# Kernel optimization log

Hardware: AMD Instinct MI355X
Metric: run time of the kernel (lower is better)

## Reference

```python
import jax, jax.numpy as jnp
import numpy as np

EPS = 1e-06
FP8_MAX = 448.0  # float8_e4m3fn max
T, H = 8192, 4096


def setup_inputs() -> dict:
    key = jax.random.key(0)
    ks = jax.random.split(key, 5)
    return {
        "hidden_states": jax.random.normal(ks[0], (T, H), dtype=jnp.float32),
        "norm_w": jax.random.uniform(ks[1], (4, H), dtype=jnp.float32),
        "w": jax.random.uniform(ks[2], (3, H, H), dtype=jnp.float32),
        "wscale": jax.random.uniform(ks[3], (3,), dtype=jnp.float32),
        "scale": jax.random.uniform(ks[4], (3,), dtype=jnp.float32),
    }


def _rmsnorm(x, g):
    var = jnp.mean(x * x, axis=-1, keepdims=True)
    return x * jax.lax.rsqrt(var + EPS) * g


def _fp8_quant(x, s):
    # static per-tensor quant: scale, clamp to fp8 range, cast to e4m3 and back
    q = jnp.clip(x / s, -FP8_MAX, FP8_MAX)
    return q.astype(jnp.float8_e4m3fn).astype(jnp.float32)


def _fp8_linear(x, wq, s_in, s_w):
    qx = _fp8_quant(x, s_in)
    return (qx @ wq) * (s_in * s_w)


def reference(hidden_states, norm_w, w, wscale, scale):
    # weight fp8 quantization (module stores weights already in fp8)
    wq = w.astype(jnp.float8_e4m3fn).astype(jnp.float32)  # [3,H,H]

    z = jax.nn.relu(hidden_states)
    x = resid = z  # all_reduce == identity on one device
    y = _rmsnorm(x, norm_w[0])

    z2 = _fp8_linear(y, wq[0], scale[0], wscale[0])
    x2 = z2 + resid
    resid = x2
    y2 = _rmsnorm(x2, norm_w[1])

    z3 = _fp8_linear(y2, wq[1], scale[1], wscale[1])
    x3 = z3 + resid
    resid = x3
    y3 = _rmsnorm(x3, norm_w[2])

    z4 = _fp8_linear(y3, wq[2], scale[2], wscale[2])
    x4 = z4 + resid
    y4 = _rmsnorm(x4, norm_w[3])
    return y4
```

## Files before the change

### kernel.cpp

```cpp
#include <hip/hip_runtime.h>

typedef float f32x4  __attribute__((ext_vector_type(4)));
typedef float f32x16 __attribute__((ext_vector_type(16)));
typedef int   i32x4  __attribute__((ext_vector_type(4)));
typedef int   i32x8  __attribute__((ext_vector_type(8)));

#define T_DIM 8192
#define H_DIM 4096
#define SC1 0x7f7f7f7f

__device__ __forceinline__ unsigned int pack_fp8x4(float a, float b, float c, float d) {
    int v = __builtin_amdgcn_cvt_pk_fp8_f32(a, b, 0, false);
    v = __builtin_amdgcn_cvt_pk_fp8_f32(c, d, v, true);
    return (unsigned int)v;
}


__global__ __launch_bounds__(256) void wquant_kernel(
    const float* __restrict__ w, unsigned char* __restrict__ wqT)
{
    const int l  = blockIdx.z;
    const int n0 = blockIdx.x * 64;
    const int k0 = blockIdx.y * 64;
    const int tid = threadIdx.x;
    __shared__ unsigned char tile[64][68];
    const float* wl = w + (size_t)l * H_DIM * H_DIM;
#pragma unroll
    for (int p = 0; p < 4; ++p) {
        int r = p * 16 + (tid >> 4);
        int c = (tid & 15) * 4;
        f32x4 v = *(const f32x4*)(wl + (size_t)(k0 + r) * H_DIM + n0 + c);
        *(unsigned int*)&tile[r][c] = pack_fp8x4(v[0], v[1], v[2], v[3]);
    }
    __syncthreads();
    const int nl = tid >> 2;
    const int g  = tid & 3;
    unsigned int words[4];
#pragma unroll
    for (int wi = 0; wi < 4; ++wi) {
        unsigned int a = 0;
#pragma unroll
        for (int b = 0; b < 4; ++b)
            a |= (unsigned int)tile[g * 16 + wi * 4 + b][nl] << (8 * b);
        words[wi] = a;
    }
    const int bn = n0 >> 8, wc = (n0 >> 6) & 3, kt = k0 >> 6;
    const int n2 = nl >> 5;
    const int lane = (g >> 1) * 32 + (nl & 31);
    const int byte0 = (g & 1) * 16;
    const size_t off = ((((size_t)l * 16 + bn) * 64 + kt) * 4 + wc) * 2 + n2;
    unsigned char* op = wqT + off * 2048 + lane * 32 + byte0;
    uint4 ov; ov.x = words[0]; ov.y = words[1]; ov.z = words[2]; ov.w = words[3];
    *(uint4*)op = ov;
}

template <int MODE>
__global__ __launch_bounds__(256) void row_kernel(
    const float* __restrict__ in,
    float* __restrict__ resid_out,
    void* __restrict__ out,
    const float* __restrict__ g,
    const float* __restrict__ scale_p)
{
    const int row = blockIdx.x;
    const int tid = threadIdx.x;
    const float* rin = in + (size_t)row * H_DIM;
    float x[16];
    float ss = 0.0f;
#pragma unroll
    for (int j = 0; j < 4; ++j) {
        const int base = (j * 256 + tid) * 4;
        f32x4 v = *(const f32x4*)(rin + base);
        f32x4 rv;
#pragma unroll
        for (int i = 0; i < 4; ++i) {
            float t = v[i];
            if (MODE == 0) t = fmaxf(t, 0.0f);
            x[j * 4 + i] = t;
            rv[i] = t;
            ss += t * t;
        }
        if (MODE == 0)
            *(f32x4*)(resid_out + (size_t)row * H_DIM + base) = rv;
    }
#pragma unroll
    for (int off = 32; off > 0; off >>= 1)
        ss += __shfl_down(ss, off, 64);
    __shared__ float red[4];
    if ((tid & 63) == 0) red[tid >> 6] = ss;
    __syncthreads();
    const float var  = (red[0] + red[1] + red[2] + red[3]) * (1.0f / (float)H_DIM);
    const float rinv = 1.0f / sqrtf(var + 1e-6f);

    if (MODE == 2) {
        float* ro = (float*)out + (size_t)row * H_DIM;
#pragma unroll
        for (int j = 0; j < 4; ++j) {
            const int base = (j * 256 + tid) * 4;
            f32x4 gv = *(const f32x4*)(g + base);
            f32x4 ov;
#pragma unroll
            for (int i = 0; i < 4; ++i) ov[i] = (x[j * 4 + i] * rinv) * gv[i];
            *(f32x4*)(ro + base) = ov;
        }
    } else {
        const float s = scale_p[0];
        unsigned int* qo = (unsigned int*)out + (size_t)row * (H_DIM / 4);
#pragma unroll
        for (int j = 0; j < 4; ++j) {
            const int base = (j * 256 + tid) * 4;
            f32x4 gv = *(const f32x4*)(g + base);
            float q[4];
#pragma unroll
            for (int i = 0; i < 4; ++i) {
                float y = (x[j * 4 + i] * rinv) * gv[i];
                y = y / s;
                q[i] = fminf(fmaxf(y, -448.0f), 448.0f);
            }
            qo[j * 256 + tid] = pack_fp8x4(q[0], q[1], q[2], q[3]);
        }
    }
}

#define LGKM0B do { asm volatile("s_waitcnt lgkmcnt(0)" ::: "memory"); \
                    __builtin_amdgcn_s_barrier(); } while (0)

#define MM2(m, P) do {                                                          \
    acc[m][0] = __builtin_amdgcn_mfma_scale_f32_32x32x64_f8f6f4(                \
        fa[m], b##P##0, acc[m][0], 0, 0, 0, SC1, 0, SC1);                       \
    acc[m][1] = __builtin_amdgcn_mfma_scale_f32_32x32x64_f8f6f4(                \
        fa[m], b##P##1, acc[m][1], 0, 0, 0, SC1, 0, SC1);                       \
} while (0)

#define RDA(ORQ, m) do {                                                        \
    *(i32x4*)&fa[m]         = *(const i32x4*)(lds + (ORQ) + wrA + (m) * 2048 + fo0); \
    *(((i32x4*)&fa[m]) + 1) = *(const i32x4*)(lds + (ORQ) + wrA + (m) * 2048 + fo1); \
} while (0)

#define AITER(WRa, WRb, LDa, LDb, FC, FN, BUF) do {                             \
    LDa = *(const i32x4*)(gAlo + kt2);                                          \
    LDb = *(const i32x4*)(gAhi + kt2);                                          \
    kt2 += 64;                                                                  \
    b##FN##0 = *(const i32x8*)(gB0 + ktb);                                      \
    b##FN##1 = *(const i32x8*)(gB0 + ktb + 2048);                               \
    ktb += 16384;                                                               \
    *(i32x4*)(lds + (BUF) + tid16)        = WRa;                                \
    *(i32x4*)(lds + (BUF) + 8192 + tid16) = WRb;                                \
    LGKM0B;                                                                     \
    __builtin_amdgcn_s_setprio(1); MM2(0, FC); MM2(1, FC);                      \
    __builtin_amdgcn_s_setprio(0);                                              \
    RDA(BUF, 0); RDA(BUF, 1);                                                   \
    __builtin_amdgcn_s_setprio(1); MM2(2, FC); MM2(3, FC);                      \
    __builtin_amdgcn_s_setprio(0);                                              \
    RDA(BUF, 2); RDA(BUF, 3);                                                   \
} while (0)

__global__ __launch_bounds__(512, 2) void gemm_fp8_kernel(
    const unsigned char* __restrict__ A,
    const unsigned char* __restrict__ B,
    float* __restrict__ C,
    const float* __restrict__ s_in,
    const float* __restrict__ s_w)
{
    __shared__ unsigned char lds[32768];

    const float alpha = s_in[0] * s_w[0];

    const int b = blockIdx.x;
    const int local = b >> 3, chunk = b & 7;
    const int bm = (chunk & 3) * 8 + (local & 7);
    const int bn = (chunk >> 2) * 8 + (local >> 3);

    const int tid  = threadIdx.x;
    const int wave = tid >> 6;
    const int lane = tid & 63;
    const int wr   = wave >> 2;
    const int wc   = wave & 3;

    const int sw  = (lane >> 1) & 3;
    const int fo0 = (lane & 31) * 64 + ((((lane >> 5) * 2) + 0 ^ sw)) * 16;
    const int fo1 = (lane & 31) * 64 + ((((lane >> 5) * 2) + 1 ^ sw)) * 16;
    const int wrA = wr * 8192;

    const int voff = (tid >> 2) * H_DIM + ((tid & 3) ^ ((tid >> 3) & 3)) * 16;
    const unsigned char* gAlo = A + (size_t)bm * 256 * H_DIM + voff;
    const unsigned char* gAhi = gAlo + (size_t)128 * H_DIM;
    const int tid16 = tid * 16;

    const unsigned char* gB0 =
        B + ((((size_t)bn * 64) * 4 + wc) * 2) * 2048 + lane * 32;

    f32x16 acc[4][2];
#pragma unroll
    for (int m = 0; m < 4; ++m)
#pragma unroll
        for (int n = 0; n < 2; ++n)
#pragma unroll
            for (int e = 0; e < 16; ++e) acc[m][n][e] = 0.0f;

    i32x8 fa[4];
    i32x4 rXa, rXb, rYa, rYb;
    i32x8 bX0, bX1, bY0, bY1;
    int kt2, ktb;

    rXa = *(const i32x4*)(gAlo);
    rXb = *(const i32x4*)(gAhi);
    bX0 = *(const i32x8*)(gB0);
    bX1 = *(const i32x8*)(gB0 + 2048);
    rYa = *(const i32x4*)(gAlo + 64);
    rYb = *(const i32x4*)(gAhi + 64);
    *(i32x4*)(lds + tid16)        = rXa;
    *(i32x4*)(lds + 8192 + tid16) = rXb;
    LGKM0B;
    RDA(0, 0); RDA(0, 1); RDA(0, 2); RDA(0, 3);
    kt2 = 128;
    ktb = 16384;

#pragma unroll 1
    for (int it = 0; it < 31; ++it) {
        AITER(rYa, rYb, rXa, rXb, X, Y, 16384);
        AITER(rXa, rXb, rYa, rYb, Y, X, 0);
    }
    bY0 = *(const i32x8*)(gB0 + ktb);
    bY1 = *(const i32x8*)(gB0 + ktb + 2048);
    *(i32x4*)(lds + 16384 + tid16)        = rYa;
    *(i32x4*)(lds + 16384 + 8192 + tid16) = rYb;
    LGKM0B;
    __builtin_amdgcn_s_setprio(1); MM2(0, X); MM2(1, X);
    __builtin_amdgcn_s_setprio(0);
    RDA(16384, 0); RDA(16384, 1);
    __builtin_amdgcn_s_setprio(1); MM2(2, X); MM2(3, X);
    __builtin_amdgcn_s_setprio(0);
    RDA(16384, 2); RDA(16384, 3);
    MM2(0, Y); MM2(1, Y); MM2(2, Y); MM2(3, Y);

    const int lrow0 = bm * 256 + wr * 128 + 4 * (lane >> 5);
    const int lcol0 = bn * 256 + wc * 64 + (lane & 31);
#pragma unroll
    for (int m = 0; m < 4; ++m) {
#pragma unroll
        for (int n = 0; n < 2; ++n) {
#pragma unroll
            for (int e = 0; e < 16; ++e) {
                const int row = lrow0 + m * 32 + (e & 3) + 8 * (e >> 2);
                float* cp = C + (size_t)row * H_DIM + lcol0 + n * 32;
                *cp = acc[m][n][e] * alpha + *cp;
            }
        }
    }
}

extern "C" void kernel_launch(void* const* d_in, const int* in_sizes, int n_in,
                              void* d_out, int out_size, void* d_ws, size_t ws_size,
                              hipStream_t stream) {
    const float* h   = (const float*)d_in[0];
    const float* nw  = (const float*)d_in[1];
    const float* w   = (const float*)d_in[2];
    const float* wsc = (const float*)d_in[3];
    const float* sc  = (const float*)d_in[4];
    float* out = (float*)d_out;

    unsigned char* wqT = (unsigned char*)d_ws;
    unsigned char* qx  = wqT + (size_t)3 * H_DIM * H_DIM;
    float* resid = (float*)(qx + (size_t)T_DIM * H_DIM);

    const size_t WSTRIDE = (size_t)H_DIM * H_DIM;

    wquant_kernel<<<dim3(64, 64, 3), 256, 0, stream>>>(w, wqT);

    row_kernel<0><<<T_DIM, 256, 0, stream>>>(h, resid, qx, nw + 0 * H_DIM, sc + 0);
    gemm_fp8_kernel<<<512, 512, 0, stream>>>(qx, wqT + 0 * WSTRIDE, resid, sc + 0, wsc + 0);

    row_kernel<1><<<T_DIM, 256, 0, stream>>>(resid, nullptr, qx, nw + 1 * H_DIM, sc + 1);
    gemm_fp8_kernel<<<512, 512, 0, stream>>>(qx, wqT + 1 * WSTRIDE, resid, sc + 1, wsc + 1);

    row_kernel<1><<<T_DIM, 256, 0, stream>>>(resid, nullptr, qx, nw + 2 * H_DIM, sc + 2);
    gemm_fp8_kernel<<<512, 512, 0, stream>>>(qx, wqT + 2 * WSTRIDE, resid, sc + 2, wsc + 2);

    row_kernel<2><<<T_DIM, 256, 0, stream>>>(resid, nullptr, out, nw + 3 * H_DIM, nullptr);
}
```

Measured before the change: 666.6 us.

## Write activations in MFMA fragment layout and load A directly to registers

The norm+quant kernel now writes fp8 activations in a tiled layout that matches the MFMA A-fragment order (32-row blocks, 64-byte K tiles split into halves). The GEMM drops the LDS staging, barriers and swizzled shared-memory reads for A and instead loads each wave's A fragments straight from global memory, the same way B is already loaded. This removes LDS traffic and block-wide synchronisation. The cost is that A tiles shared across the four column waves are now fetched redundantly from global or L2, and there is no longer a software prefetch buffer hiding load latency.

```diff
diff --git a/kernel.cpp b/kernel.cpp
--- a/kernel.cpp
+++ b/kernel.cpp
@@ -105,7 +105,8 @@
         }
     } else {
         const float s = scale_p[0];
-        unsigned int* qo = (unsigned int*)out + (size_t)row * (H_DIM / 4);
+        unsigned int* qo = (unsigned int*)out;
+        const int mrow = row >> 5, rl = row & 31;
 #pragma unroll
         for (int j = 0; j < 4; ++j) {
             const int base = (j * 256 + tid) * 4;
@@ -117,13 +118,14 @@
                 y = y / s;
                 q[i] = fminf(fmaxf(y, -448.0f), 448.0f);
             }
-            qo[j * 256 + tid] = pack_fp8x4(q[0], q[1], q[2], q[3]);
-        }
-    }
-}
-
-#define LGKM0B do { asm volatile("s_waitcnt lgkmcnt(0)" ::: "memory"); \
-                    __builtin_amdgcn_s_barrier(); } while (0)
+            const int W  = j * 256 + tid;
+            const int kt = W >> 4, kh = (W >> 3) & 1, wb = W & 7;
+            const size_t widx =
+                (((size_t)mrow * 64 + kt) * 64 + (kh * 32 + rl)) * 8 + wb;
+            qo[widx] = pack_fp8x4(q[0], q[1], q[2], q[3]);
+        }
+    }
+}
 
 #define MM2(m, P) do {                                                          \
     acc[m][0] = __builtin_amdgcn_mfma_scale_f32_32x32x64_f8f6f4(                \
@@ -132,27 +134,15 @@
         fa[m], b##P##1, acc[m][1], 0, 0, 0, SC1, 0, SC1);                       \
 } while (0)
 
-#define RDA(ORQ, m) do {                                                        \
-    *(i32x4*)&fa[m]         = *(const i32x4*)(lds + (ORQ) + wrA + (m) * 2048 + fo0); \
-    *(((i32x4*)&fa[m]) + 1) = *(const i32x4*)(lds + (ORQ) + wrA + (m) * 2048 + fo1); \
-} while (0)
-
-#define AITER(WRa, WRb, LDa, LDb, FC, FN, BUF) do {                             \
-    LDa = *(const i32x4*)(gAlo + kt2);                                          \
-    LDb = *(const i32x4*)(gAhi + kt2);                                          \
-    kt2 += 64;                                                                  \
-    b##FN##0 = *(const i32x8*)(gB0 + ktb);                                      \
-    b##FN##1 = *(const i32x8*)(gB0 + ktb + 2048);                               \
-    ktb += 16384;                                                               \
-    *(i32x4*)(lds + (BUF) + tid16)        = WRa;                                \
-    *(i32x4*)(lds + (BUF) + 8192 + tid16) = WRb;                                \
-    LGKM0B;                                                                     \
-    __builtin_amdgcn_s_setprio(1); MM2(0, FC); MM2(1, FC);                      \
-    __builtin_amdgcn_s_setprio(0);                                              \
-    RDA(BUF, 0); RDA(BUF, 1);                                                   \
-    __builtin_amdgcn_s_setprio(1); MM2(2, FC); MM2(3, FC);                      \
-    __builtin_amdgcn_s_setprio(0);                                              \
-    RDA(BUF, 2); RDA(BUF, 3);                                                   \
+#define TILE(P) do {                                                            \
+    MM2(0, P); fa[0] = *(const i32x8*)(gAm0 + ka);                              \
+    MM2(1, P); fa[1] = *(const i32x8*)(gAm1 + ka);                              \
+    MM2(2, P); fa[2] = *(const i32x8*)(gAm2 + ka);                              \
+    MM2(3, P); fa[3] = *(const i32x8*)(gAm3 + ka);                              \
+    ka += 2048;                                                                 \
+    b##P##0 = *(const i32x8*)(gB0 + kb);                                        \
+    b##P##1 = *(const i32x8*)(gB0 + kb + 2048);                                 \
+    kb += 16384;                                                                \
 } while (0)
 
 __global__ __launch_bounds__(512, 2) void gemm_fp8_kernel(
@@ -162,8 +152,6 @@
     const float* __restrict__ s_in,
     const float* __restrict__ s_w)
 {
-    __shared__ unsigned char lds[32768];
-
     const float alpha = s_in[0] * s_w[0];
 
     const int b = blockIdx.x;
@@ -177,18 +165,13 @@
     const int wr   = wave >> 2;
     const int wc   = wave & 3;
 
-    const int sw  = (lane >> 1) & 3;
-    const int fo0 = (lane & 31) * 64 + ((((lane >> 5) * 2) + 0 ^ sw)) * 16;
-    const int fo1 = (lane & 31) * 64 + ((((lane >> 5) * 2) + 1 ^ sw)) * 16;
-    const int wrA = wr * 8192;
-
-    const int voff = (tid >> 2) * H_DIM + ((tid & 3) ^ ((tid >> 3) & 3)) * 16;
-    const unsigned char* gAlo = A + (size_t)bm * 256 * H_DIM + voff;
-    const unsigned char* gAhi = gAlo + (size_t)128 * H_DIM;
-    const int tid16 = tid * 16;
-
+    const unsigned char* gAm0 =
+        A + ((size_t)(bm * 8 + wr * 4) * 64) * 2048 + lane * 32;
+    const unsigned char* gAm1 = gAm0 + 131072;
+    const unsigned char* gAm2 = gAm0 + 2 * 131072;
+    const unsigned char* gAm3 = gAm0 + 3 * 131072;
     const unsigned char* gB0 =
-        B + ((((size_t)bn * 64) * 4 + wc) * 2) * 2048 + lane * 32;
+        B + (((size_t)bn * 256 + wc) * 2) * 2048 + lane * 32;
 
     f32x16 acc[4][2];
 #pragma unroll
@@ -198,40 +181,28 @@
 #pragma unroll
             for (int e = 0; e < 16; ++e) acc[m][n][e] = 0.0f;
 
-    i32x8 fa[4];
-    i32x4 rXa, rXb, rYa, rYb;
-    i32x8 bX0, bX1, bY0, bY1;
-    int kt2, ktb;
-
-    rXa = *(const i32x4*)(gAlo);
-    rXb = *(const i32x4*)(gAhi);
+    i32x8 fa[4], bX0, bX1, bY0, bY1;
+
+    fa[0] = *(const i32x8*)(gAm0);
+    fa[1] = *(const i32x8*)(gAm1);
+    fa[2] = *(const i32x8*)(gAm2);
+    fa[3] = *(const i32x8*)(gAm3);
     bX0 = *(const i32x8*)(gB0);
     bX1 = *(const i32x8*)(gB0 + 2048);
-    rYa = *(const i32x4*)(gAlo + 64);
-    rYb = *(const i32x4*)(gAhi + 64);
-    *(i32x4*)(lds + tid16)        = rXa;
-    *(i32x4*)(lds + 8192 + tid16) = rXb;
-    LGKM0B;
-    RDA(0, 0); RDA(0, 1); RDA(0, 2); RDA(0, 3);
-    kt2 = 128;
-    ktb = 16384;
+    bY0 = *(const i32x8*)(gB0 + 16384);
+    bY1 = *(const i32x8*)(gB0 + 16384 + 2048);
+    int ka = 2048;
+    int kb = 2 * 16384;
 
 #pragma unroll 1
     for (int it = 0; it < 31; ++it) {
-        AITER(rYa, rYb, rXa, rXb, X, Y, 16384);
-        AITER(rXa, rXb, rYa, rYb, Y, X, 0);
-    }
-    bY0 = *(const i32x8*)(gB0 + ktb);
-    bY1 = *(const i32x8*)(gB0 + ktb + 2048);
-    *(i32x4*)(lds + 16384 + tid16)        = rYa;
-    *(i32x4*)(lds + 16384 + 8192 + tid16) = rYb;
-    LGKM0B;
-    __builtin_amdgcn_s_setprio(1); MM2(0, X); MM2(1, X);
-    __builtin_amdgcn_s_setprio(0);
-    RDA(16384, 0); RDA(16384, 1);
-    __builtin_amdgcn_s_setprio(1); MM2(2, X); MM2(3, X);
-    __builtin_amdgcn_s_setprio(0);
-    RDA(16384, 2); RDA(16384, 3);
+        TILE(X);
+        TILE(Y);
+    }
+    MM2(0, X); fa[0] = *(const i32x8*)(gAm0 + ka);
+    MM2(1, X); fa[1] = *(const i32x8*)(gAm1 + ka);
+    MM2(2, X); fa[2] = *(const i32x8*)(gAm2 + ka);
+    MM2(3, X); fa[3] = *(const i32x8*)(gAm3 + ka);
     MM2(0, Y); MM2(1, Y); MM2(2, Y); MM2(3, Y);
 
     const int lrow0 = bm * 256 + wr * 128 + 4 * (lane >> 5);
```

After: 743.9 us. +11.6%, slower.

## Triple-buffer A tiles in LDS with one barrier per k-step, preload residual

Applied to the files above, without the earlier changes.

Grows LDS from two to three A buffers so that writing the next tile and reading the current one go to different buffers. This allows a single waitcnt+barrier at the end of each k-step instead of one before the MFMAs, and MFMA/LDS-read pairs are interleaved more finely. The residual from C is now loaded into the accumulators (divided by alpha) before the main loop rather than read-modify-written in the epilogue. The larger LDS footprint at 2 blocks per CU and the extra up-front global loads may limit occupancy, and pre-dividing by alpha can change rounding slightly.

```diff
diff --git a/kernel.cpp b/kernel.cpp
--- a/kernel.cpp
+++ b/kernel.cpp
@@ -122,8 +122,9 @@
     }
 }
 
-#define LGKM0B do { asm volatile("s_waitcnt lgkmcnt(0)" ::: "memory"); \
-                    __builtin_amdgcn_s_barrier(); } while (0)
+#define BUF0 0
+#define BUF1 16384
+#define BUF2 32768
 
 #define MM2(m, P) do {                                                          \
     acc[m][0] = __builtin_amdgcn_mfma_scale_f32_32x32x64_f8f6f4(                \
@@ -137,22 +138,23 @@
     *(((i32x4*)&fa[m]) + 1) = *(const i32x4*)(lds + (ORQ) + wrA + (m) * 2048 + fo1); \
 } while (0)
 
-#define AITER(WRa, WRb, LDa, LDb, FC, FN, BUF) do {                             \
-    LDa = *(const i32x4*)(gAlo + kt2);                                          \
-    LDb = *(const i32x4*)(gAhi + kt2);                                          \
-    kt2 += 64;                                                                  \
-    b##FN##0 = *(const i32x8*)(gB0 + ktb);                                      \
-    b##FN##1 = *(const i32x8*)(gB0 + ktb + 2048);                               \
-    ktb += 16384;                                                               \
-    *(i32x4*)(lds + (BUF) + tid16)        = WRa;                                \
-    *(i32x4*)(lds + (BUF) + 8192 + tid16) = WRb;                                \
-    LGKM0B;                                                                     \
-    __builtin_amdgcn_s_setprio(1); MM2(0, FC); MM2(1, FC);                      \
-    __builtin_amdgcn_s_setprio(0);                                              \
-    RDA(BUF, 0); RDA(BUF, 1);                                                   \
-    __builtin_amdgcn_s_setprio(1); MM2(2, FC); MM2(3, FC);                      \
-    __builtin_amdgcn_s_setprio(0);                                              \
-    RDA(BUF, 2); RDA(BUF, 3);                                                   \
+#define ITER(WR, LD, FC, FN, BUFW, BUFR) do {                                   \
+    r##LD##a = *(const i32x4*)(gAlo + ka);                                      \
+    r##LD##b = *(const i32x4*)(gAhi + ka); ka += 64;                            \
+    b##FN##0 = *(const i32x8*)(gB0 + kb);                                       \
+    b##FN##1 = *(const i32x8*)(gB0 + kb + 2048); kb += 16384;                   \
+    *(i32x4*)(lds + (BUFW) + tid16)        = r##WR##a;                          \
+    *(i32x4*)(lds + (BUFW) + 8192 + tid16) = r##WR##b;                          \
+    __builtin_amdgcn_s_setprio(1); MM2(0, FC); __builtin_amdgcn_s_setprio(0);   \
+    RDA(BUFR, 0);                                                               \
+    __builtin_amdgcn_s_setprio(1); MM2(1, FC); __builtin_amdgcn_s_setprio(0);   \
+    RDA(BUFR, 1);                                                               \
+    __builtin_amdgcn_s_setprio(1); MM2(2, FC); __builtin_amdgcn_s_setprio(0);   \
+    RDA(BUFR, 2);                                                               \
+    __builtin_amdgcn_s_setprio(1); MM2(3, FC); __builtin_amdgcn_s_setprio(0);   \
+    RDA(BUFR, 3);                                                               \
+    asm volatile("s_waitcnt lgkmcnt(0)" ::: "memory");                          \
+    __builtin_amdgcn_s_barrier();                                               \
 } while (0)
 
 __global__ __launch_bounds__(512, 2) void gemm_fp8_kernel(
@@ -162,9 +164,10 @@
     const float* __restrict__ s_in,
     const float* __restrict__ s_w)
 {
-    __shared__ unsigned char lds[32768];
-
-    const float alpha = s_in[0] * s_w[0];
+    __shared__ unsigned char lds[49152];
+
+    const float alpha  = s_in[0] * s_w[0];
+    const float ralpha = 1.0f / alpha;
 
     const int b = blockIdx.x;
     const int local = b >> 3, chunk = b & 7;
@@ -190,52 +193,79 @@
     const unsigned char* gB0 =
         B + ((((size_t)bn * 64) * 4 + wc) * 2) * 2048 + lane * 32;
 
+    const int lrow0 = bm * 256 + wr * 128 + 4 * (lane >> 5);
+    const int lcol0 = bn * 256 + wc * 64 + (lane & 31);
+
     f32x16 acc[4][2];
 #pragma unroll
     for (int m = 0; m < 4; ++m)
 #pragma unroll
         for (int n = 0; n < 2; ++n)
 #pragma unroll
-            for (int e = 0; e < 16; ++e) acc[m][n][e] = 0.0f;
+            for (int e = 0; e < 16; ++e) {
+                const int row = lrow0 + m * 32 + (e & 3) + 8 * (e >> 2);
+                acc[m][n][e] =
+                    C[(size_t)row * H_DIM + lcol0 + n * 32] * ralpha;
+            }
 
     i32x8 fa[4];
     i32x4 rXa, rXb, rYa, rYb;
     i32x8 bX0, bX1, bY0, bY1;
-    int kt2, ktb;
 
     rXa = *(const i32x4*)(gAlo);
     rXb = *(const i32x4*)(gAhi);
+    rYa = *(const i32x4*)(gAlo + 64);
+    rYb = *(const i32x4*)(gAhi + 64);
+    *(i32x4*)(lds + BUF0 + tid16)        = rXa;
+    *(i32x4*)(lds + BUF0 + 8192 + tid16) = rXb;
+    *(i32x4*)(lds + BUF1 + tid16)        = rYa;
+    *(i32x4*)(lds + BUF1 + 8192 + tid16) = rYb;
+    rXa = *(const i32x4*)(gAlo + 128);
+    rXb = *(const i32x4*)(gAhi + 128);
     bX0 = *(const i32x8*)(gB0);
     bX1 = *(const i32x8*)(gB0 + 2048);
-    rYa = *(const i32x4*)(gAlo + 64);
-    rYb = *(const i32x4*)(gAhi + 64);
-    *(i32x4*)(lds + tid16)        = rXa;
-    *(i32x4*)(lds + 8192 + tid16) = rXb;
-    LGKM0B;
-    RDA(0, 0); RDA(0, 1); RDA(0, 2); RDA(0, 3);
-    kt2 = 128;
-    ktb = 16384;
+    asm volatile("s_waitcnt lgkmcnt(0)" ::: "memory");
+    __builtin_amdgcn_s_barrier();
+    RDA(BUF0, 0); RDA(BUF0, 1); RDA(BUF0, 2); RDA(BUF0, 3);
+    int ka = 192;
+    int kb = 16384;
 
 #pragma unroll 1
-    for (int it = 0; it < 31; ++it) {
-        AITER(rYa, rYb, rXa, rXb, X, Y, 16384);
-        AITER(rXa, rXb, rYa, rYb, Y, X, 0);
-    }
-    bY0 = *(const i32x8*)(gB0 + ktb);
-    bY1 = *(const i32x8*)(gB0 + ktb + 2048);
-    *(i32x4*)(lds + 16384 + tid16)        = rYa;
-    *(i32x4*)(lds + 16384 + 8192 + tid16) = rYb;
-    LGKM0B;
-    __builtin_amdgcn_s_setprio(1); MM2(0, X); MM2(1, X);
-    __builtin_amdgcn_s_setprio(0);
-    RDA(16384, 0); RDA(16384, 1);
-    __builtin_amdgcn_s_setprio(1); MM2(2, X); MM2(3, X);
-    __builtin_amdgcn_s_setprio(0);
-    RDA(16384, 2); RDA(16384, 3);
+    for (int it = 0; it < 10; ++it) {
+        ITER(X, Y, X, Y, BUF2, BUF1);
+        ITER(Y, X, Y, X, BUF0, BUF2);
+        ITER(X, Y, X, Y, BUF1, BUF0);
+        ITER(Y, X, Y, X, BUF2, BUF1);
+        ITER(X, Y, X, Y, BUF0, BUF2);
+        ITER(Y, X, Y, X, BUF1, BUF0);
+    }
+    ITER(X, Y, X, Y, BUF2, BUF1);
+    bX0 = *(const i32x8*)(gB0 + kb);
+    bX1 = *(const i32x8*)(gB0 + kb + 2048); kb += 16384;
+    *(i32x4*)(lds + BUF0 + tid16)        = rYa;
+    *(i32x4*)(lds + BUF0 + 8192 + tid16) = rYb;
+    __builtin_amdgcn_s_setprio(1); MM2(0, Y); __builtin_amdgcn_s_setprio(0);
+    RDA(BUF2, 0);
+    __builtin_amdgcn_s_setprio(1); MM2(1, Y); __builtin_amdgcn_s_setprio(0);
+    RDA(BUF2, 1);
+    __builtin_amdgcn_s_setprio(1); MM2(2, Y); __builtin_amdgcn_s_setprio(0);
+    RDA(BUF2, 2);
+    __builtin_amdgcn_s_setprio(1); MM2(3, Y); __builtin_amdgcn_s_setprio(0);
+    RDA(BUF2, 3);
+    asm volatile("s_waitcnt lgkmcnt(0)" ::: "memory");
+    __builtin_amdgcn_s_barrier();
+    bY0 = *(const i32x8*)(gB0 + kb);
+    bY1 = *(const i32x8*)(gB0 + kb + 2048);
+    __builtin_amdgcn_s_setprio(1); MM2(0, X); __builtin_amdgcn_s_setprio(0);
+    RDA(BUF0, 0);
+    __builtin_amdgcn_s_setprio(1); MM2(1, X); __builtin_amdgcn_s_setprio(0);
+    RDA(BUF0, 1);
+    __builtin_amdgcn_s_setprio(1); MM2(2, X); __builtin_amdgcn_s_setprio(0);
+    RDA(BUF0, 2);
+    __builtin_amdgcn_s_setprio(1); MM2(3, X); __builtin_amdgcn_s_setprio(0);
+    RDA(BUF0, 3);
     MM2(0, Y); MM2(1, Y); MM2(2, Y); MM2(3, Y);
 
-    const int lrow0 = bm * 256 + wr * 128 + 4 * (lane >> 5);
-    const int lcol0 = bn * 256 + wc * 64 + (lane & 31);
 #pragma unroll
     for (int m = 0; m < 4; ++m) {
 #pragma unroll
@@ -243,8 +273,7 @@
 #pragma unroll
             for (int e = 0; e < 16; ++e) {
                 const int row = lrow0 + m * 32 + (e & 3) + 8 * (e >> 2);
-                float* cp = C + (size_t)row * H_DIM + lcol0 + n * 32;
-                *cp = acc[m][n][e] * alpha + *cp;
+                C[(size_t)row * H_DIM + lcol0 + n * 32] = acc[m][n][e] * alpha;
             }
         }
     }
```

Result: slower. 1.156 ms (+73.5%).
